# Kernel tuning notes

Hardware: AMD Instinct MI355X
Metric: run time of the kernel (lower is better)

The kernel has to match this reference:

```python
import jax, jax.numpy as jnp
import numpy as np

L, H, NH, NKV, HD, FF, V = 2, 2048, 16, 2, 128, 11008, 32000
B, S, R, LORA_SCALE = 32, 64, 16, 2.0  # lora scaling = alpha/r = 32/16
PH, TD = 1024, 512
ROPE_THETA = 1e6

def _rms(x, w, eps=1e-6):
    return x * jax.lax.rsqrt(jnp.mean(x * x, axis=-1, keepdims=True) + eps) * w

def _rot_half(x):
    h = x.shape[-1] // 2
    return jnp.concatenate([-x[..., h:], x[..., :h]], axis=-1)

def _lora_linear(x, W, A, Bm, b=None):
    y = x @ W.T + LORA_SCALE * ((x @ A.T) @ Bm.T)
    return y + b if b is not None else y

def _forward(input_ids, attention_mask, embed, Wq, bq, Aq, Bq, Wk, bk, Ak, Bk,
             Wv, bv, Av, Bv, Wo, Ao, Bo, ln1, ln2, Wg, Wu, Wd, norm_f,
             W1, b1, W2, b2):
    Bsz, Sl = input_ids.shape
    h = embed[input_ids]                                            # [B,S,H]
    inv_freq = 1.0 / (ROPE_THETA ** (jnp.arange(0, HD, 2, dtype=jnp.float32) / HD))
    ang = jnp.arange(Sl, dtype=jnp.float32)[:, None] * inv_freq      # [S,HD/2]
    cos = jnp.concatenate([jnp.cos(ang)] * 2, -1)[None, :, None, :]  # [1,S,1,HD]
    sin = jnp.concatenate([jnp.sin(ang)] * 2, -1)[None, :, None, :]
    causal = jnp.tril(jnp.ones((Sl, Sl), dtype=bool))
    keep = causal[None, None] & (attention_mask[:, None, None, :] > 0)
    bias = jnp.where(keep, 0.0, -1e9).astype(jnp.float32)            # [B,1,S,S]
    for l in range(L):
        x = _rms(h, ln1[l])
        q = _lora_linear(x, Wq[l], Aq[l], Bq[l], bq[l]).reshape(Bsz, Sl, NH, HD)
        k = _lora_linear(x, Wk[l], Ak[l], Bk[l], bk[l]).reshape(Bsz, Sl, NKV, HD)
        v = _lora_linear(x, Wv[l], Av[l], Bv[l], bv[l]).reshape(Bsz, Sl, NKV, HD)
        q = q * cos + _rot_half(q) * sin
        k = k * cos + _rot_half(k) * sin
        k = jnp.repeat(k, NH // NKV, axis=2)                         # GQA expand
        v = jnp.repeat(v, NH // NKV, axis=2)
        scores = jnp.einsum('bqhd,bkhd->bhqk', q, k) / np.sqrt(HD).astype(np.float32) + bias
        p = jax.nn.softmax(scores, axis=-1)
        attn = jnp.einsum('bhqk,bkhd->bqhd', p, v).reshape(Bsz, Sl, H)
        h = h + _lora_linear(attn, Wo[l], Ao[l], Bo[l])
        x = _rms(h, ln2[l])
        h = h + (jax.nn.silu(x @ Wg[l].T) * (x @ Wu[l].T)) @ Wd[l].T  # SwiGLU MLP
    h = _rms(h, norm_f)                       # final norm -> hidden_states[-1]
    seq_len = jnp.sum(attention_mask, axis=1) - 1
    pooled = h[jnp.arange(Bsz), seq_len]      # last valid token  [B,H]
    z = jax.nn.gelu(pooled @ W1.T + b1, approximate=False)
    return (z @ W2.T + b2).astype(jnp.float32)  # [B,512]

def setup_inputs():
    key = jax.random.key(0)
    ks = jax.random.split(key, 32)
    def n(k, shape, s=0.02):
        return (s * jax.random.normal(k, shape)).astype(jnp.float32)
    lens = jax.random.randint(ks[0], (B,), 1, S + 1)
    return {
        'input_ids': jax.random.randint(ks[1], (B, S), 0, V, dtype=jnp.int32),
        'attention_mask': (jnp.arange(S)[None, :] < lens[:, None]).astype(jnp.int32),
        'embed': n(ks[2], (V, H)),
        'Wq': n(ks[3], (L, H, H)), 'bq': n(ks[4], (L, H)),
        'Aq': n(ks[5], (L, R, H)), 'Bq': n(ks[6], (L, H, R)),
        'Wk': n(ks[7], (L, NKV * HD, H)), 'bk': n(ks[8], (L, NKV * HD)),
        'Ak': n(ks[9], (L, R, H)), 'Bk': n(ks[10], (L, NKV * HD, R)),
        'Wv': n(ks[11], (L, NKV * HD, H)), 'bv': n(ks[12], (L, NKV * HD)),
        'Av': n(ks[13], (L, R, H)), 'Bv': n(ks[14], (L, NKV * HD, R)),
        'Wo': n(ks[15], (L, H, H)),
        'Ao': n(ks[16], (L, R, H)), 'Bo': n(ks[17], (L, H, R)),
        'ln1': jnp.ones((L, H), jnp.float32), 'ln2': jnp.ones((L, H), jnp.float32),
        'Wg': n(ks[18], (L, FF, H)), 'Wu': n(ks[19], (L, FF, H)), 'Wd': n(ks[20], (L, H, FF)),
        'norm_f': jnp.ones((H,), jnp.float32),
        'W1': n(ks[21], (PH, H)), 'b1': jnp.zeros((PH,), jnp.float32),
        'W2': n(ks[22], (TD, PH)), 'b2': jnp.zeros((TD,), jnp.float32),
    }

def reference(input_ids, attention_mask, embed, Wq, bq, Aq, Bq, Wk, bk, Ak, Bk,
              Wv, bv, Av, Bv, Wo, Ao, Bo, ln1, ln2, Wg, Wu, Wd, norm_f,
              W1, b1, W2, b2):
    return _forward(input_ids, attention_mask, embed, Wq, bq, Aq, Bq, Wk, bk, Ak, Bk,
                    Wv, bv, Av, Bv, Wo, Ao, Bo, ln1, ln2, Wg, Wu, Wd, norm_f,
                    W1, b1, W2, b2)
```

## Files before the change

kernel.cpp:

```cpp
#include <hip/hip_runtime.h>
#include <hip/hip_bf16.h>
#include <math.h>

namespace {
constexpr int NL  = 2;
constexpr int H   = 2048;
constexpr int NH  = 16;
constexpr int NKV = 2;
constexpr int HD  = 128;
constexpr int FF  = 11008;
constexpr int BB  = 32;
constexpr int SS  = 64;
constexpr int RR  = 16;
constexpr int TT  = BB * SS;
constexpr int KVD = NKV * HD;
constexpr int QKVD = H + 2 * KVD;
constexpr int PH  = 1024, TDm = 512;
constexpr float LSCALE = 2.0f;
}

typedef __bf16 bf16x8 __attribute__((ext_vector_type(8)));
typedef float  f32x4  __attribute__((ext_vector_type(4)));

__device__ __forceinline__ ushort4 f4_to_bf4(float4 r) {
  __hip_bfloat16 a = __float2bfloat16(r.x), b = __float2bfloat16(r.y),
                 c = __float2bfloat16(r.z), d = __float2bfloat16(r.w);
  return make_ushort4(*(unsigned short*)&a, *(unsigned short*)&b,
                      *(unsigned short*)&c, *(unsigned short*)&d);
}

__device__ __forceinline__ bf16x8 f8cvt(float4 a, float4 b) {
  bf16x8 r;
  r[0] = (__bf16)a.x; r[1] = (__bf16)a.y; r[2] = (__bf16)a.z; r[3] = (__bf16)a.w;
  r[4] = (__bf16)b.x; r[5] = (__bf16)b.y; r[6] = (__bf16)b.z; r[7] = (__bf16)b.w;
  return r;
}

__device__ __forceinline__ float dot4(float4 a, float4 b) {
  return a.x * b.x + a.y * b.y + a.z * b.z + a.w * b.w;
}

__global__ __launch_bounds__(256) void k_embed(const int* __restrict__ ids,
                                               const float* __restrict__ emb,
                                               float* __restrict__ h) {
  int t = blockIdx.x;
  long id = ids[t];
  const float4* src = reinterpret_cast<const float4*>(emb + id * (long)H);
  float4* dst = reinterpret_cast<float4*>(h + (long)t * H);
  for (int i = threadIdx.x; i < H / 4; i += 256) dst[i] = src[i];
}

__global__ __launch_bounds__(256) void k_prep(
    const float* __restrict__ bq, const float* __restrict__ bk, const float* __restrict__ bv,
    const float* __restrict__ Bq, const float* __restrict__ Bk, const float* __restrict__ Bv,
    float* __restrict__ biascat, float* __restrict__ bcat) {
  int idx = blockIdx.x * 256 + threadIdx.x;
  if (idx >= NL * QKVD) return;
  int l = idx / QKVD, col = idx % QKVD;
  const float* bsrc; const float* Bsrc;
  if (col < H)            { bsrc = bq + (long)l * H + col;            Bsrc = Bq + ((long)l * H + col) * RR; }
  else if (col < H + KVD) { bsrc = bk + (long)l * KVD + (col - H);    Bsrc = Bk + ((long)l * KVD + col - H) * RR; }
  else                    { bsrc = bv + (long)l * KVD + (col - H - KVD); Bsrc = Bv + ((long)l * KVD + col - H - KVD) * RR; }
  biascat[idx] = *bsrc;
  #pragma unroll
  for (int r = 0; r < RR; ++r) bcat[(long)idx * RR + r] = Bsrc[r];
}

__global__ __launch_bounds__(256) void k_rmsnorm(const float* __restrict__ in,
                                                 const float* __restrict__ w,
                                                 float* __restrict__ out,
                                                 __hip_bfloat16* __restrict__ outb) {
  int t = blockIdx.x, tid = threadIdx.x;
  const float4* xr = reinterpret_cast<const float4*>(in + (long)t * H);
  float4 v0 = xr[tid], v1 = xr[tid + 256];
  float ss = v0.x*v0.x + v0.y*v0.y + v0.z*v0.z + v0.w*v0.w
           + v1.x*v1.x + v1.y*v1.y + v1.z*v1.z + v1.w*v1.w;
  #pragma unroll
  for (int off = 32; off; off >>= 1) ss += __shfl_xor(ss, off);
  __shared__ float sred[4];
  if ((tid & 63) == 0) sred[tid >> 6] = ss;
  __syncthreads();
  float scale = rsqrtf((sred[0] + sred[1] + sred[2] + sred[3]) * (1.0f / H) + 1e-6f);
  const float4* wr = reinterpret_cast<const float4*>(w);
  float4 w0 = wr[tid], w1 = wr[tid + 256];
  float4 r0 = make_float4(v0.x*scale*w0.x, v0.y*scale*w0.y, v0.z*scale*w0.z, v0.w*scale*w0.w);
  float4 r1 = make_float4(v1.x*scale*w1.x, v1.y*scale*w1.y, v1.z*scale*w1.z, v1.w*scale*w1.w);
  float4* o = reinterpret_cast<float4*>(out + (long)t * H);
  o[tid] = r0; o[tid + 256] = r1;
  ushort4* ob = reinterpret_cast<ushort4*>(outb + (long)t * H);
  ob[tid] = f4_to_bf4(r0); ob[tid + 256] = f4_to_bf4(r1);
}

enum { ME_BIAS_F32 = 0, ME_ACC_F32 = 1 };

__device__ __forceinline__ int raster_sw(int bid, int nwg) {
  int q8 = nwg >> 3, r8 = nwg & 7;
  int xcd = bid & 7, pos = bid >> 3;
  return (xcd < r8 ? xcd * (q8 + 1) : r8 * (q8 + 1) + (xcd - r8) * q8) + pos;
}

template <int EPI, bool LORA>
__global__ __launch_bounds__(256, 3) void k_mgemm(
    const __hip_bfloat16* __restrict__ Abf,
    const float* __restrict__ W0, const float* __restrict__ W1, const float* __restrict__ W2,
    const float* __restrict__ bias,
    float* __restrict__ Cf,
    const float* __restrict__ lt, const float* __restrict__ lB, int ltStride,
    int qkvMode, int M, int N, int K) {
  constexpr int BM = 64, BN = 128, BK = 64;
  constexpr int FM = 4, FN = 2;
  __shared__ __align__(16) __bf16 As[2][BM * BK];
  __shared__ __align__(16) __bf16 Bs[2][BN * BK];
  const int tid = threadIdx.x;
  const int sw = raster_sw(blockIdx.x, gridDim.x);
  const int ntm = M / BM;
  const int bm = (sw % ntm) * BM, bn = (sw / ntm) * BN;
  const int lane = tid & 63, wv = tid >> 6;
  const int wn = wv * 32;
  const int lr15 = lane & 15;
  const int g4 = lane >> 4;
  f32x4 acc[FM][FN] = {};
  const __bf16* Ag = reinterpret_cast<const __bf16*>(Abf) + (long)bm * K;

  const float* Wsrc = W0; int wrow0 = bn;
  if (qkvMode) {
    if (bn >= H + KVD)      { Wsrc = W2; wrow0 = bn - (H + KVD); }
    else if (bn >= H)       { Wsrc = W1; wrow0 = bn - H; }
  }

  const int arow = tid >> 3, acol = tid & 7;

  auto stageA = [&](int buf, int k0) {
    __builtin_amdgcn_global_load_lds(
        (const __attribute__((address_space(1))) void*)
          (Ag + (long)arow * K + k0 + ((acol ^ (arow & 7)) << 3)),
        (__attribute__((address_space(3))) void*)(&As[buf][tid * 8]), 16, 0, 0);
    int r1 = arow + 32;
    __builtin_amdgcn_global_load_lds(
        (const __attribute__((address_space(1))) void*)
          (Ag + (long)r1 * K + k0 + ((acol ^ (r1 & 7)) << 3)),
        (__attribute__((address_space(3))) void*)(&As[buf][(tid + 256) * 8]), 16, 0, 0);
  };

  float4 bb[4][2];
  auto loadB = [&](int k0) {
    #pragma unroll
    for (int q = 0; q < 4; ++q) {
      int r = arow + q * 32;
      const float* p = Wsrc + (long)(wrow0 + r) * K + k0 + ((acol ^ (r & 7)) << 3);
      bb[q][0] = *reinterpret_cast<const float4*>(p);
      bb[q][1] = *reinterpret_cast<const float4*>(p + 4);
    }
  };
  auto writeB = [&](int buf) {
    #pragma unroll
    for (int q = 0; q < 4; ++q)
      *reinterpret_cast<bf16x8*>(&Bs[buf][(tid + q * 256) * 8]) = f8cvt(bb[q][0], bb[q][1]);
  };
  auto compute = [&](int buf) {
    #pragma unroll
    for (int ks = 0; ks < 2; ++ks) {
      bf16x8 af[FM], bfr[FN];
      #pragma unroll
      for (int m = 0; m < FM; ++m) {
        int row = m * 16 + lr15;
        af[m] = *reinterpret_cast<const bf16x8*>(
            &As[buf][row * BK + (((g4 + 4 * ks) ^ (row & 7)) << 3)]);
      }
      #pragma unroll
      for (int n = 0; n < FN; ++n) {
        int row = wn + n * 16 + lr15;
        bfr[n] = *reinterpret_cast<const bf16x8*>(
            &Bs[buf][row * BK + (((g4 + 4 * ks) ^ (row & 7)) << 3)]);
      }
      #pragma unroll
      for (int m = 0; m < FM; ++m)
        #pragma unroll
        for (int n = 0; n < FN; ++n)
          acc[m][n] = __builtin_amdgcn_mfma_f32_16x16x32_bf16(af[m], bfr[n], acc[m][n], 0, 0, 0);
    }
  };

  const int NS = K / BK;
  loadB(0);
  stageA(0, 0);
  writeB(0);
  __syncthreads();
  int cur = 0;
  for (int t = 0; t < NS; ++t) {
    if (t + 1 < NS) { loadB((t + 1) * BK); stageA(cur ^ 1, (t + 1) * BK); }
    compute(cur);
    if (t + 1 < NS) {
      writeB(cur ^ 1);
      __syncthreads();
      cur ^= 1;
    }
  }

  const int r0 = g4 << 2;
  float4 lb[FN][4];
  int goff = 0;
  if constexpr (LORA) {
    if (qkvMode) goff = (bn >= H + KVD) ? 32 : (bn >= H ? 16 : 0);
    #pragma unroll
    for (int n = 0; n < FN; ++n) {
      const float4* p = reinterpret_cast<const float4*>(lB + (long)(bn + wn + n * 16 + lr15) * RR);
      lb[n][0] = p[0]; lb[n][1] = p[1]; lb[n][2] = p[2]; lb[n][3] = p[3];
    }
  }
  float bcol[FN];
  if constexpr (EPI == ME_BIAS_F32) {
    #pragma unroll
    for (int n = 0; n < FN; ++n) bcol[n] = bias[bn + wn + n * 16 + lr15];
  }
  #pragma unroll
  for (int m = 0; m < FM; ++m)
    #pragma unroll
    for (int j = 0; j < 4; ++j) {
      const long row = bm + m * 16 + r0 + j;
      float lv[FN];
      if constexpr (LORA) {
        const float4* tp = reinterpret_cast<const float4*>(lt + row * ltStride + goff);
        float4 t0 = tp[0], t1 = tp[1], t2 = tp[2], t3 = tp[3];
        #pragma unroll
        for (int n = 0; n < FN; ++n)
          lv[n] = LSCALE * (dot4(t0, lb[n][0]) + dot4(t1, lb[n][1]) +
                            dot4(t2, lb[n][2]) + dot4(t3, lb[n][3]));
      }
      #pragma unroll
      for (int n = 0; n < FN; ++n) {
        const int col = bn + wn + n * 16 + lr15;
        float v = acc[m][n][j];
        if constexpr (LORA) v += lv[n];
        if constexpr (EPI == ME_BIAS_F32) Cf[row * N + col] = v + bcol[n];
        else                              Cf[row * N + col] += v;
      }
    }
}

__global__ __launch_bounds__(256, 2) void k_swiglu(
    const __hip_bfloat16* __restrict__ Abf,
    const float* __restrict__ Wg,
    const float* __restrict__ Wu,
    __hip_bfloat16* __restrict__ Cb,
    int M, int N, int K) {
  constexpr int BM = 128, BN = 128, BK = 32;
  constexpr int FM = 4, FN = 4;
  __shared__ __align__(16) __bf16 As[2][BM * BK];
  __shared__ __align__(16) __bf16 Gs[2][BN * BK];
  __shared__ __align__(16) __bf16 Us[2][BN * BK];
  const int tid = threadIdx.x;
  const int sw = raster_sw(blockIdx.x, gridDim.x);
  const int ntm = M / BM;
  const int bm = (sw % ntm) * BM, bn = (sw / ntm) * BN;
  const int lane = tid & 63, wv = tid >> 6;
  const int wm = (wv >> 1) * 64, wn = (wv & 1) * 64;
  const int lr15 = lane & 15;
  const int lks = (((lane >> 4) << 3)) ^ ((((lr15 >> 1) & 3)) << 3);
  f32x4 accg[FM][FN] = {}, accu[FM][FN] = {};
  const __bf16* Ag = reinterpret_cast<const __bf16*>(Abf) + (long)bm * K;

  const int br0 = tid >> 2, bc = tid & 3;
  const int br1 = br0 + 64;
  const float* gp0 = Wg + (long)(bn + br0) * K + bc * 8;
  const float* gp1 = Wg + (long)(bn + br1) * K + bc * 8;
  const float* up0 = Wu + (long)(bn + br0) * K + bc * 8;
  const float* up1 = Wu + (long)(bn + br1) * K + bc * 8;
  const int d0 = br0 * BK + ((bc ^ ((br0 >> 1) & 3)) << 3);
  const int d1 = br1 * BK + ((bc ^ ((br1 >> 1) & 3)) << 3);

  float4 g00, g01, g10, g11, u00, u01, u10, u11;
  auto loadB = [&](int k0) {
    g00 = *reinterpret_cast<const float4*>(gp0 + k0);
    g01 = *reinterpret_cast<const float4*>(gp0 + k0 + 4);
    g10 = *reinterpret_cast<const float4*>(gp1 + k0);
    g11 = *reinterpret_cast<const float4*>(gp1 + k0 + 4);
    u00 = *reinterpret_cast<const float4*>(up0 + k0);
    u01 = *reinterpret_cast<const float4*>(up0 + k0 + 4);
    u10 = *reinterpret_cast<const float4*>(up1 + k0);
    u11 = *reinterpret_cast<const float4*>(up1 + k0 + 4);
  };
  auto writeB = [&](int buf) {
    *reinterpret_cast<bf16x8*>(&Gs[buf][d0]) = f8cvt(g00, g01);
    *reinterpret_cast<bf16x8*>(&Gs[buf][d1]) = f8cvt(g10, g11);
    *reinterpret_cast<bf16x8*>(&Us[buf][d0]) = f8cvt(u00, u01);
    *reinterpret_cast<bf16x8*>(&Us[buf][d1]) = f8cvt(u10, u11);
  };
  auto stageA = [&](int buf, int k0) {
    #pragma unroll
    for (int i = tid; i < BM * BK / 8; i += 256)
      __builtin_amdgcn_global_load_lds(
          (const __attribute__((address_space(1))) void*)
            (Ag + (long)(i >> 2) * K + k0 + (((i & 3) ^ ((i >> 3) & 3)) << 3)),
          (__attribute__((address_space(3))) void*)(&As[buf][i * 8]), 16, 0, 0);
  };
  auto compute = [&](int buf) {
    bf16x8 af[FM], gf[FN], uf[FN];
    #pragma unroll
    for (int m = 0; m < FM; ++m)
      af[m] = *reinterpret_cast<const bf16x8*>(&As[buf][(wm + m * 16 + lr15) * BK + lks]);
    #pragma unroll
    for (int n = 0; n < FN; ++n) {
      gf[n] = *reinterpret_cast<const bf16x8*>(&Gs[buf][(wn + n * 16 + lr15) * BK + lks]);
      uf[n] = *reinterpret_cast<const bf16x8*>(&Us[buf][(wn + n * 16 + lr15) * BK + lks]);
    }
    #pragma unroll
    for (int m = 0; m < FM; ++m)
      #pragma unroll
      for (int n = 0; n < FN; ++n) {
        accg[m][n] = __builtin_amdgcn_mfma_f32_16x16x32_bf16(af[m], gf[n], accg[m][n], 0, 0, 0);
        accu[m][n] = __builtin_amdgcn_mfma_f32_16x16x32_bf16(af[m], uf[n], accu[m][n], 0, 0, 0);
      }
  };

  const int NS = K / BK;
  loadB(0);
  stageA(0, 0);
  writeB(0);
  __syncthreads();
  int cur = 0;
  for (int t = 0; t < NS; ++t) {
    if (t + 1 < NS) { loadB((t + 1) * BK); stageA(cur ^ 1, (t + 1) * BK); }
    compute(cur);
    if (t + 1 < NS) {
      writeB(cur ^ 1);
      __syncthreads();
      cur ^= 1;
    }
  }

  const int r0 = (lane >> 4) << 2;
  #pragma unroll
  for (int m = 0; m < FM; ++m)
    #pragma unroll
    for (int n = 0; n < FN; ++n) {
      const int col = bn + wn + n * 16 + lr15;
      const long rowb = bm + wm + m * 16 + r0;
      #pragma unroll
      for (int j = 0; j < 4; ++j) {
        float g = accg[m][n][j], u = accu[m][n][j];
        Cb[(rowb + j) * N + col] = __float2bfloat16((g / (1.0f + expf(-g))) * u);
      }
    }
}

enum { EPI_STORE = 0, EPI_GELU = 3 };

template <int EPI, bool HAS_BIAS>
__global__ __launch_bounds__(256) void k_gemm(const float* __restrict__ A,
                                              const float* __restrict__ W,
                                              const float* __restrict__ bias,
                                              float* __restrict__ C,
                                              int M, int N, int K) {
  constexpr int BM = 64, BN = 64, BK = 16;
  __shared__ float As[BK][BM + 4];
  __shared__ float Ws[BK][BN + 4];
  const int bm = blockIdx.y * BM, bn = blockIdx.x * BN;
  const int tid = threadIdx.x;
  const int lr = tid >> 2;
  const int lc = (tid & 3) << 2;
  const int ty = tid >> 4, tx = tid & 15;
  float acc[4][4] = {};
  const int arow = bm + lr;
  const bool aok = arow < M;
  const float* Ap = A + (long)arow * K + lc;
  const float* Wp = W + (long)(bn + lr) * K + lc;
  for (int k0 = 0; k0 < K; k0 += BK) {
    float4 av = aok ? *reinterpret_cast<const float4*>(Ap + k0) : make_float4(0.f, 0.f, 0.f, 0.f);
    float4 wv = *reinterpret_cast<const float4*>(Wp + k0);
    As[lc + 0][lr] = av.x; As[lc + 1][lr] = av.y; As[lc + 2][lr] = av.z; As[lc + 3][lr] = av.w;
    Ws[lc + 0][lr] = wv.x; Ws[lc + 1][lr] = wv.y; Ws[lc + 2][lr] = wv.z; Ws[lc + 3][lr] = wv.w;
    __syncthreads();
    #pragma unroll
    for (int k = 0; k < BK; ++k) {
      float4 a4 = *reinterpret_cast<const float4*>(&As[k][ty << 2]);
      float4 b4 = *reinterpret_cast<const float4*>(&Ws[k][tx << 2]);
      float a[4] = {a4.x, a4.y, a4.z, a4.w};
      float b[4] = {b4.x, b4.y, b4.z, b4.w};
      #pragma unroll
      for (int i = 0; i < 4; ++i)
        #pragma unroll
        for (int j = 0; j < 4; ++j) acc[i][j] = fmaf(a[i], b[j], acc[i][j]);
    }
    __syncthreads();
  }
  const int col = bn + (tx << 2);
  #pragma unroll
  for (int i = 0; i < 4; ++i) {
    int row = bm + (ty << 2) + i;
    if (row < M) {
      float4 r = make_float4(acc[i][0], acc[i][1], acc[i][2], acc[i][3]);
      if (HAS_BIAS) {
        float4 bv = *reinterpret_cast<const float4*>(bias + col);
        r.x += bv.x; r.y += bv.y; r.z += bv.z; r.w += bv.w;
      }
      if (EPI == EPI_GELU) {
        r.x = 0.5f * r.x * (1.0f + erff(r.x * 0.70710678118654752f));
        r.y = 0.5f * r.y * (1.0f + erff(r.y * 0.70710678118654752f));
        r.z = 0.5f * r.z * (1.0f + erff(r.z * 0.70710678118654752f));
        r.w = 0.5f * r.w * (1.0f + erff(r.w * 0.70710678118654752f));
      }
      *reinterpret_cast<float4*>(C + (long)row * N + col) = r;
    }
  }
}

__global__ __launch_bounds__(256) void k_lora_down3(
    const float* __restrict__ x,
    const float* __restrict__ A0, const float* __restrict__ A1, const float* __restrict__ A2,
    float* __restrict__ out, int outStride) {
  int t = blockIdx.x, g = blockIdx.y, tid = threadIdx.x;
  const float* A = (g == 0) ? A0 : (g == 1) ? A1 : A2;
  int r = tid & 15, sl = tid >> 4;
  const float* xr = x + (long)t * H + sl * 128;
  const float* Ar = A + (long)r * H + sl * 128;
  float p = 0.f;
  #pragma unroll 8
  for (int kk = 0; kk < 128; kk += 4) {
    float4 xv = *reinterpret_cast<const float4*>(xr + kk);
    float4 av = *reinterpret_cast<const float4*>(Ar + kk);
    p = fmaf(xv.x, av.x, p); p = fmaf(xv.y, av.y, p);
    p = fmaf(xv.z, av.z, p); p = fmaf(xv.w, av.w, p);
  }
  __shared__ float red[16][17];
  red[sl][r] = p;
  __syncthreads();
  if (tid < 16) {
    float s = 0.f;
    #pragma unroll
    for (int i = 0; i < 16; ++i) s += red[i][tid];
    out[(long)t * outStride + g * 16 + tid] = s;
  }
}

__global__ __launch_bounds__(256) void k_rope_tab(float2* __restrict__ tab) {
  int idx = blockIdx.x * 256 + threadIdx.x;
  if (idx >= SS * 64) return;
  int pos = idx >> 6, j = idx & 63;
  float inv = 1.0f / powf(1.0e6f, (float)(2 * j) * (1.0f / HD));
  float ang = (float)pos * inv;
  tab[idx] = make_float2(cosf(ang), sinf(ang));
}

__global__ __launch_bounds__(256) void k_rope(float* __restrict__ qkv,
                                              const float2* __restrict__ tab) {
  int t = blockIdx.x;
  const float2* trow = tab + (t & (SS - 1)) * 64;
  float* row = qkv + (long)t * QKVD;
  for (int idx = threadIdx.x; idx < NH * 64 + NKV * 64; idx += 256) {
    float* base;
    int j;
    if (idx < NH * 64) {
      int head = idx >> 6; j = idx & 63;
      base = row + head * HD;
    } else {
      int i2 = idx - NH * 64;
      int head = i2 >> 6; j = i2 & 63;
      base = row + H + head * HD;
    }
    float2 cs2 = trow[j];
    float lo = base[j], hi = base[j + 64];
    base[j]      = lo * cs2.x - hi * cs2.y;
    base[j + 64] = hi * cs2.x + lo * cs2.y;
  }
}

__global__ __launch_bounds__(64) void k_attn(const float* __restrict__ qkv,
                                             const int* __restrict__ mask,
                                             float* __restrict__ o,
                                             __hip_bfloat16* __restrict__ obf) {
  int flat = blockIdx.x;
  int qi = flat & (SS - 1);
  int hh = (flat >> 6) & (NH - 1);
  int b  = flat >> 10;
  int lane = threadIdx.x;
  int kv = hh >> 3;
  long t = (long)b * SS + qi;
  const float* qr = qkv + t * QKVD + hh * HD;
  const float* kr = qkv + ((long)b * SS + lane) * QKVD + H + kv * HD;
  float dot = 0.f;
  #pragma unroll 8
  for (int d = 0; d < HD; d += 4) {
    float4 qv = *reinterpret_cast<const float4*>(qr + d);
    float4 kvv = *reinterpret_cast<const float4*>(kr + d);
    dot = fmaf(qv.x, kvv.x, dot); dot = fmaf(qv.y, kvv.y, dot);
    dot = fmaf(qv.z, kvv.z, dot); dot = fmaf(qv.w, kvv.w, dot);
  }
  bool keep = (lane <= qi) && (mask[b * SS + lane] > 0);
  float sc = dot * 0.08838834764831845f + (keep ? 0.f : -1e9f);
  float m = sc;
  #pragma unroll
  for (int off = 32; off; off >>= 1) m = fmaxf(m, __shfl_xor(m, off));
  float e = expf(sc - m);
  float s = e;
  #pragma unroll
  for (int off = 32; off; off >>= 1) s += __shfl_xor(s, off);
  float p = e / s;
  __shared__ float pl[64];
  pl[lane] = p;
  __syncthreads();
  float o0 = 0.f, o1 = 0.f;
  const float* vb = qkv + (long)b * SS * QKVD + H + KVD + kv * HD;
  for (int ki = 0; ki < SS; ++ki) {
    float pp = pl[ki];
    o0 = fmaf(pp, vb[(long)ki * QKVD + lane], o0);
    o1 = fmaf(pp, vb[(long)ki * QKVD + lane + 64], o1);
  }
  long oidx = t * H + hh * HD + lane;
  o[oidx] = o0;
  o[oidx + 64] = o1;
  __hip_bfloat16 b0 = __float2bfloat16(o0), b1 = __float2bfloat16(o1);
  obf[oidx] = b0;
  obf[oidx + 64] = b1;
}

__global__ __launch_bounds__(256) void k_pool(const float* __restrict__ x,
                                              const int* __restrict__ mask,
                                              float* __restrict__ pooled) {
  int b = blockIdx.x;
  __shared__ int len;
  if (threadIdx.x == 0) {
    int L2 = 0;
    for (int i = 0; i < SS; ++i) L2 += (mask[b * SS + i] > 0);
    len = L2;
  }
  __syncthreads();
  const float4* sp = reinterpret_cast<const float4*>(x + ((long)b * SS + len - 1) * H);
  float4* dp = reinterpret_cast<float4*>(pooled + (long)b * H);
  for (int i = threadIdx.x; i < H / 4; i += 256) dp[i] = sp[i];
}

extern "C" void kernel_launch(void* const* d_in, const int* in_sizes, int n_in,
                              void* d_out, int out_size, void* d_ws, size_t ws_size,
                              hipStream_t stream) {
  const int*   ids    = (const int*)d_in[0];
  const int*   mask   = (const int*)d_in[1];
  const float* embed  = (const float*)d_in[2];
  const float* Wq     = (const float*)d_in[3];
  const float* bq     = (const float*)d_in[4];
  const float* Aq     = (const float*)d_in[5];
  const float* Bq     = (const float*)d_in[6];
  const float* Wk     = (const float*)d_in[7];
  const float* bk     = (const float*)d_in[8];
  const float* Ak     = (const float*)d_in[9];
  const float* Bk     = (const float*)d_in[10];
  const float* Wv     = (const float*)d_in[11];
  const float* bv     = (const float*)d_in[12];
  const float* Av     = (const float*)d_in[13];
  const float* Bv     = (const float*)d_in[14];
  const float* Wo     = (const float*)d_in[15];
  const float* Ao     = (const float*)d_in[16];
  const float* Bo     = (const float*)d_in[17];
  const float* ln1    = (const float*)d_in[18];
  const float* ln2    = (const float*)d_in[19];
  const float* Wg     = (const float*)d_in[20];
  const float* Wu     = (const float*)d_in[21];
  const float* Wd     = (const float*)d_in[22];
  const float* norm_f = (const float*)d_in[23];
  const float* W1     = (const float*)d_in[24];
  const float* b1     = (const float*)d_in[25];
  const float* W2     = (const float*)d_in[26];
  const float* b2     = (const float*)d_in[27];

  float* ws = (float*)d_ws;
  float* h        = ws;
  float* x        = h    + (long)TT * H;
  float* qkv      = x    + (long)TT * H;
  float* tmpR     = qkv  + (long)TT * QKVD;
  float* tmpO     = tmpR + (long)TT * 48;
  float* pooled   = tmpO + (long)TT * 16;
  float* zz       = pooled + (long)BB * H;
  float* biascat  = zz   + (long)BB * PH;
  float* bcat     = biascat + (long)NL * QKVD;
  float2* ropetab = (float2*)(bcat + (long)NL * QKVD * RR);
  float* endf32   = (float*)(ropetab + SS * 64);
  __hip_bfloat16* x_bf = (__hip_bfloat16*)endf32;
  __hip_bfloat16* ffbf = x_bf + (long)TT * H;

  k_embed<<<TT, 256, 0, stream>>>(ids, embed, h);
  k_rope_tab<<<(SS * 64 + 255) / 256, 256, 0, stream>>>(ropetab);
  k_prep<<<(NL * QKVD + 255) / 256, 256, 0, stream>>>(bq, bk, bv, Bq, Bk, Bv, biascat, bcat);

  for (int l = 0; l < NL; ++l) {
    const long lHH = (long)l * H * H;
    const long lKH = (long)l * KVD * H;
    const long lRH = (long)l * RR * H;
    const long lFH = (long)l * FF * H;
    k_rmsnorm<<<TT, 256, 0, stream>>>(h, ln1 + l * H, x, x_bf);
    k_lora_down3<<<dim3(TT, 3), 256, 0, stream>>>(
        x, Aq + lRH, Ak + lRH, Av + lRH, tmpR, 48);
    k_mgemm<ME_BIAS_F32, true><<<(TT / 64) * (QKVD / 128), 256, 0, stream>>>(
        x_bf, Wq + lHH, Wk + lKH, Wv + lKH, biascat + (long)l * QKVD, qkv,
        tmpR, bcat + (long)l * QKVD * RR, 48, 1, TT, QKVD, H);
    k_rope<<<TT, 256, 0, stream>>>(qkv, ropetab);
    k_attn<<<BB * NH * SS, 64, 0, stream>>>(qkv, mask, x, x_bf);
    k_lora_down3<<<dim3(TT, 1), 256, 0, stream>>>(
        x, Ao + lRH, Ao + lRH, Ao + lRH, tmpO, 16);
    k_mgemm<ME_ACC_F32, true><<<(TT / 64) * (H / 128), 256, 0, stream>>>(
        x_bf, Wo + lHH, Wo + lHH, Wo + lHH, nullptr, h,
        tmpO, Bo + (long)l * H * RR, 16, 0, TT, H, H);
    k_rmsnorm<<<TT, 256, 0, stream>>>(h, ln2 + l * H, x, x_bf);
    k_swiglu<<<(TT / 128) * (FF / 128), 256, 0, stream>>>(
        x_bf, Wg + lFH, Wu + lFH, ffbf, TT, FF, H);
    k_mgemm<ME_ACC_F32, false><<<(TT / 64) * (H / 128), 256, 0, stream>>>(
        ffbf, Wd + lFH, Wd + lFH, Wd + lFH, nullptr, h,
        nullptr, nullptr, 0, 0, TT, H, FF);
  }

  k_rmsnorm<<<TT, 256, 0, stream>>>(h, norm_f, x, x_bf);
  k_pool<<<BB, 256, 0, stream>>>(x, mask, pooled);
  k_gemm<EPI_GELU, true><<<dim3(PH / 64, 1), 256, 0, stream>>>(pooled, W1, b1, zz, BB, PH, H);
  k_gemm<EPI_STORE, true><<<dim3(TDm / 64, 1), 256, 0, stream>>>(zz, W2, b2, (float*)d_out, BB, TDm, PH);
}
```

Measured before the change: 2.171 ms.

## Pre-convert SwiGLU weights to bf16 and use async LDS-load 512-thread kernel

Adds a conversion kernel that turns the fp32 gate and up weights into bf16 in workspace each layer. A new SwiGLU GEMM then streams A and both weight tiles straight into LDS with global_load_lds. It uses a three-stage buffer, a 128x256 tile with 512 threads, and swizzled layout. This is meant to remove the per-tile fp32-to-bf16 conversion and register staging in the main loop. The cost is two extra full passes over the weights each call and larger LDS and register use, and it falls back to the old path if the workspace is too small.

Measured after the change: 2.290 ms. 1.05x slower.

```diff
diff --git a/kernel.cpp b/kernel.cpp
--- a/kernel.cpp
+++ b/kernel.cpp
@@ -48,6 +48,14 @@
   const float4* src = reinterpret_cast<const float4*>(emb + id * (long)H);
   float4* dst = reinterpret_cast<float4*>(h + (long)t * H);
   for (int i = threadIdx.x; i < H / 4; i += 256) dst[i] = src[i];
+}
+
+__global__ __launch_bounds__(256) void k_cvt(const float* __restrict__ src,
+                                             __hip_bfloat16* __restrict__ dst, long n) {
+  long i = ((long)blockIdx.x * 256 + threadIdx.x) * 4;
+  if (i >= n) return;
+  float4 v = *reinterpret_cast<const float4*>(src + i);
+  *reinterpret_cast<ushort4*>(dst + i) = f4_to_bf4(v);
 }
 
 __global__ __launch_bounds__(256) void k_prep(
@@ -234,6 +242,106 @@
         if constexpr (LORA) v += lv[n];
         if constexpr (EPI == ME_BIAS_F32) Cf[row * N + col] = v + bcol[n];
         else                              Cf[row * N + col] += v;
+      }
+    }
+}
+
+__global__ __launch_bounds__(512, 1) void k_swiglu8(
+    const __hip_bfloat16* __restrict__ Abf,
+    const __hip_bfloat16* __restrict__ Wgb,
+    const __hip_bfloat16* __restrict__ Wub,
+    __hip_bfloat16* __restrict__ Cb,
+    int M, int N, int K) {
+  constexpr int BM = 128, BN = 256, SL = 32;
+  constexpr int FM = 4, FN = 4;
+  __shared__ __align__(16) __bf16 As[3][BM * SL];
+  __shared__ __align__(16) __bf16 Gs[3][BN * SL];
+  __shared__ __align__(16) __bf16 Us[3][BN * SL];
+  const int tid = threadIdx.x;
+  const int sw = raster_sw(blockIdx.x, gridDim.x);
+  const int ntm = M / BM;
+  const int bm = (sw % ntm) * BM, bn = (sw / ntm) * BN;
+  const int lane = tid & 63, wid = tid >> 6;
+  const int wr = wid >> 2, wc = wid & 3;
+  const int lr15 = lane & 15;
+  const int g4 = lane >> 4;
+  const int lks = (g4 << 3) ^ (((lr15 >> 1) & 3) << 3);
+  f32x4 accg[FM][FN] = {}, accu[FM][FN] = {};
+  const __bf16* Ag = reinterpret_cast<const __bf16*>(Abf) + (long)bm * K;
+  const __bf16* Gg = reinterpret_cast<const __bf16*>(Wgb) + (long)bn * K;
+  const __bf16* Ug = reinterpret_cast<const __bf16*>(Wub) + (long)bn * K;
+
+  const int ar = tid >> 2, ac = tid & 3;
+  const int br = ar + 128;
+
+  auto stage = [&](int s, int t) {
+    const int k0 = t * SL;
+    const int sca = (ac ^ ((ar >> 1) & 3)) << 3;
+    const int scb = (ac ^ ((br >> 1) & 3)) << 3;
+    __builtin_amdgcn_global_load_lds(
+        (const __attribute__((address_space(1))) void*)(Ag + (long)ar * K + k0 + sca),
+        (__attribute__((address_space(3))) void*)(&As[s][tid * 8]), 16, 0, 0);
+    __builtin_amdgcn_global_load_lds(
+        (const __attribute__((address_space(1))) void*)(Gg + (long)ar * K + k0 + sca),
+        (__attribute__((address_space(3))) void*)(&Gs[s][tid * 8]), 16, 0, 0);
+    __builtin_amdgcn_global_load_lds(
+        (const __attribute__((address_space(1))) void*)(Gg + (long)br * K + k0 + scb),
+        (__attribute__((address_space(3))) void*)(&Gs[s][(tid + 512) * 8]), 16, 0, 0);
+    __builtin_amdgcn_global_load_lds(
+        (const __attribute__((address_space(1))) void*)(Ug + (long)ar * K + k0 + sca),
+        (__attribute__((address_space(3))) void*)(&Us[s][tid * 8]), 16, 0, 0);
+    __builtin_amdgcn_global_load_lds(
+        (const __attribute__((address_space(1))) void*)(Ug + (long)br * K + k0 + scb),
+        (__attribute__((address_space(3))) void*)(&Us[s][(tid + 512) * 8]), 16, 0, 0);
+  };
+  auto compute = [&](int s) {
+    bf16x8 af[FM], gf[FN], uf[FN];
+    #pragma unroll
+    for (int m = 0; m < FM; ++m)
+      af[m] = *reinterpret_cast<const bf16x8*>(&As[s][(wr * 64 + m * 16 + lr15) * SL + lks]);
+    #pragma unroll
+    for (int n = 0; n < FN; ++n) {
+      const int rc = wc * 64 + n * 16 + lr15;
+      gf[n] = *reinterpret_cast<const bf16x8*>(&Gs[s][rc * SL + lks]);
+      uf[n] = *reinterpret_cast<const bf16x8*>(&Us[s][rc * SL + lks]);
+    }
+    __builtin_amdgcn_s_setprio(1);
+    #pragma unroll
+    for (int m = 0; m < FM; ++m)
+      #pragma unroll
+      for (int n = 0; n < FN; ++n) {
+        accg[m][n] = __builtin_amdgcn_mfma_f32_16x16x32_bf16(af[m], gf[n], accg[m][n], 0, 0, 0);
+        accu[m][n] = __builtin_amdgcn_mfma_f32_16x16x32_bf16(af[m], uf[n], accu[m][n], 0, 0, 0);
+      }
+    __builtin_amdgcn_s_setprio(0);
+  };
+
+  const int NS = K / SL;
+  stage(0, 0);
+  stage(1, 1);
+  asm volatile("s_waitcnt vmcnt(5)" ::: "memory");
+  __builtin_amdgcn_s_barrier();
+  for (int t = 0; t < NS; ++t) {
+    if (t + 2 < NS) stage((t + 2) % 3, t + 2);
+    compute(t % 3);
+    if (t + 1 < NS) {
+      if (t + 2 < NS) asm volatile("s_waitcnt vmcnt(5)" ::: "memory");
+      else            asm volatile("s_waitcnt vmcnt(0)" ::: "memory");
+      __builtin_amdgcn_s_barrier();
+    }
+  }
+
+  const int r0 = g4 << 2;
+  #pragma unroll
+  for (int m = 0; m < FM; ++m)
+    #pragma unroll
+    for (int n = 0; n < FN; ++n) {
+      const int col = bn + wc * 64 + n * 16 + lr15;
+      const long rowb = bm + wr * 64 + m * 16 + r0;
+      #pragma unroll
+      for (int j = 0; j < 4; ++j) {
+        float g = accg[m][n][j], u = accu[m][n][j];
+        Cb[(rowb + j) * N + col] = __float2bfloat16((g / (1.0f + expf(-g))) * u);
       }
     }
 }
@@ -529,6 +637,8 @@
   float4* dp = reinterpret_cast<float4*>(pooled + (long)b * H);
   for (int i = threadIdx.x; i < H / 4; i += 256) dp[i] = sp[i];
 }
+
+static inline int cvt_grid(long n) { return (int)((n / 4 + 255) / 256); }
 
 extern "C" void kernel_launch(void* const* d_in, const int* in_sizes, int n_in,
                               void* d_out, int out_size, void* d_ws, size_t ws_size,
@@ -576,6 +686,10 @@
   float* endf32   = (float*)(ropetab + SS * 64);
   __hip_bfloat16* x_bf = (__hip_bfloat16*)endf32;
   __hip_bfloat16* ffbf = x_bf + (long)TT * H;
+  __hip_bfloat16* wbf  = ffbf + (long)TT * FF;
+  __hip_bfloat16* wbf2 = wbf  + (long)FF * H;
+  size_t need8 = (size_t)((char*)(wbf2 + (long)FF * H) - (char*)d_ws);
+  bool use8 = ws_size >= need8;
 
   k_embed<<<TT, 256, 0, stream>>>(ids, embed, h);
   k_rope_tab<<<(SS * 64 + 255) / 256, 256, 0, stream>>>(ropetab);
@@ -600,8 +714,15 @@
         x_bf, Wo + lHH, Wo + lHH, Wo + lHH, nullptr, h,
         tmpO, Bo + (long)l * H * RR, 16, 0, TT, H, H);
     k_rmsnorm<<<TT, 256, 0, stream>>>(h, ln2 + l * H, x, x_bf);
-    k_swiglu<<<(TT / 128) * (FF / 128), 256, 0, stream>>>(
-        x_bf, Wg + lFH, Wu + lFH, ffbf, TT, FF, H);
+    if (use8) {
+      k_cvt<<<cvt_grid((long)FF * H), 256, 0, stream>>>(Wg + lFH, wbf, (long)FF * H);
+      k_cvt<<<cvt_grid((long)FF * H), 256, 0, stream>>>(Wu + lFH, wbf2, (long)FF * H);
+      k_swiglu8<<<(TT / 128) * (FF / 256), 512, 0, stream>>>(
+          x_bf, wbf, wbf2, ffbf, TT, FF, H);
+    } else {
+      k_swiglu<<<(TT / 128) * (FF / 128), 256, 0, stream>>>(
+          x_bf, Wg + lFH, Wu + lFH, ffbf, TT, FF, H);
+    }
     k_mgemm<ME_ACC_F32, false><<<(TT / 64) * (H / 128), 256, 0, stream>>>(
         ffbf, Wd + lFH, Wd + lFH, Wd + lFH, nullptr, h,
         nullptr, nullptr, 0, 0, TT, H, FF);
```
